# Optimization experiments

Hardware: AMD Instinct MI355X
Metric: run time of the kernel (lower is better)

## Reference

```python
import jax, jax.numpy as jnp
import numpy as np

N = 10000       # nodes
E = 160000      # edges (avg degree 16)
IN_C = 16       # node in_channels
IN_E = 8        # edge in_edge_channels
DIMS = [32, 16, 16, 16]   # hidden_dims
ENN_H = 128     # edge_nn_hidden
EMLP_H = 16     # edge_mlp_hidden


def setup_inputs() -> dict:
    key = jax.random.key(0)
    ks = iter(jax.random.split(key, 80))
    def rn(shape, s=0.1):
        return jax.random.normal(next(ks), shape, dtype=jnp.float32) * s
    inp = {}
    inp['x'] = jax.random.normal(next(ks), (N, IN_C), dtype=jnp.float32)
    inp['edge_attr'] = jax.random.normal(next(ks), (E, IN_E), dtype=jnp.float32)
    inp['edge_index'] = jax.random.randint(next(ks), (2, E), 0, N, dtype=jnp.int32)
    in_dims = [IN_C] + DIMS[:-1]
    for i, (di, do) in enumerate(zip(in_dims, DIMS)):
        inp[f'p_w{i}'] = rn((do, di));            inp[f'p_b{i}'] = rn((do,))
        inp[f'e1_w{i}'] = rn((ENN_H, IN_E));      inp[f'e1_b{i}'] = rn((ENN_H,))
        inp[f'e2_w{i}'] = rn((do * do, ENN_H), 0.02); inp[f'e2_b{i}'] = rn((do * do,), 0.02)
        inp[f'r_w{i}'] = rn((do, do));            inp[f'c_b{i}'] = rn((do,))
    inp['m_w0'] = rn((EMLP_H, DIMS[-1])); inp['m_b0'] = rn((EMLP_H,))
    inp['m_w1'] = rn((1, EMLP_H));        inp['m_b1'] = rn((1,))
    return inp


def _forward(x, edge_attr, edge_index, params, m_w0, m_b0, m_w1, m_b1):
    row, col = edge_index[0], edge_index[1]
    n = x.shape[0]
    # in-degree for scatter-mean (clamped to 1, as PyG scatter mean)
    deg = jnp.clip(jax.ops.segment_sum(jnp.ones(row.shape[0], jnp.float32), col, num_segments=n), 1.0)
    for (pw, pb, ew1, eb1, ew2, eb2, rw, cb) in params:
        d = pw.shape[0]
        x_proj = x @ pw.T + pb                                    # [N, d]
        # edge-conditioned weight matrices: [E, d, d]
        W = (jax.nn.relu(edge_attr @ ew1.T + eb1) @ ew2.T + eb2).reshape(-1, d, d)
        msg = jnp.einsum('ei,eio->eo', x_proj[row], W)            # [E, d]
        agg = jax.ops.segment_sum(msg, col, num_segments=n) / deg[:, None]
        conv = agg + x_proj @ rw.T + cb                           # NNConv: aggr + root + bias
        x = jax.nn.relu(conv) + x_proj                            # relu + skip
    edge_repr = x[row] + x[col]                                   # [E, d_last]
    out = jax.nn.relu(edge_repr @ m_w0.T + m_b0) @ m_w1.T + m_b1  # [E, 1]
    return out[:, 0]


def reference(x, edge_attr, edge_index,
              p_w0, p_b0, e1_w0, e1_b0, e2_w0, e2_b0, r_w0, c_b0,
              p_w1, p_b1, e1_w1, e1_b1, e2_w1, e2_b1, r_w1, c_b1,
              p_w2, p_b2, e1_w2, e1_b2, e2_w2, e2_b2, r_w2, c_b2,
              p_w3, p_b3, e1_w3, e1_b3, e2_w3, e2_b3, r_w3, c_b3,
              m_w0, m_b0, m_w1, m_b1):
    params = [
        (p_w0, p_b0, e1_w0, e1_b0, e2_w0, e2_b0, r_w0, c_b0),
        (p_w1, p_b1, e1_w1, e1_b1, e2_w1, e2_b1, r_w1, c_b1),
        (p_w2, p_b2, e1_w2, e1_b2, e2_w2, e2_b2, r_w2, c_b2),
        (p_w3, p_b3, e1_w3, e1_b3, e2_w3, e2_b3, r_w3, c_b3),
    ]
    return _forward(x, edge_attr, edge_index, params, m_w0, m_b0, m_w1, m_b1)
```

## Files before the change

kernel.cpp:

```cpp
#include <hip/hip_runtime.h>

#define NN 10000
#define NE 160000
static constexpr int TPB = 256;
static constexpr int SCAN_T = 1024;

typedef unsigned int uint32;

static __device__ __forceinline__ ushort f2bf(float f) {
  uint32 u = __float_as_uint(f);
  u += 0x7fff + ((u >> 16) & 1);
  return (ushort)(u >> 16);
}
static __device__ __forceinline__ uint32 pk2bf(float a, float b) {
  return (uint32)f2bf(a) | ((uint32)f2bf(b) << 16);
}
static __device__ __forceinline__ float bflo(uint32 u) {
  return __uint_as_float(u << 16);
}
static __device__ __forceinline__ float bfhi(uint32 u) {
  return __uint_as_float(u & 0xffff0000u);
}
static __device__ __forceinline__ void dot2bf(float& acc, uint32 a, uint32 b) {
  asm("v_dot2_f32_bf16 %0, %1, %2, %0" : "+v"(acc) : "v"(a), "v"(b));
}


__global__ void k_count(const int* __restrict__ ei, int* __restrict__ cnt) {
  int e = blockIdx.x * TPB + threadIdx.x;
  if (e >= NE) return;
  atomicAdd(&cnt[ei[e]], 1);
  atomicAdd(&cnt[NN + ei[NE + e]], 1);
}

__global__ void __launch_bounds__(SCAN_T)
k_scan2(const int* __restrict__ cnt_all, int* __restrict__ off_r, int* __restrict__ cur_r,
        int* __restrict__ off_c, int* __restrict__ cur_c) {
  const int* cnt = (blockIdx.x == 0) ? cnt_all : cnt_all + NN;
  int* off = (blockIdx.x == 0) ? off_r : off_c;
  int* cur = (blockIdx.x == 0) ? cur_r : cur_c;
  __shared__ int s_wave[16];
  __shared__ int s_carry;
  int tid = threadIdx.x;
  int lane = tid & 63, wid = tid >> 6;
  if (tid == 0) s_carry = 0;
  __syncthreads();
  for (int base = 0; base < NN; base += SCAN_T) {
    int i = base + tid;
    int v = (i < NN) ? cnt[i] : 0;
    int s = v;
    #pragma unroll
    for (int d = 1; d < 64; d <<= 1) {
      int t = __shfl_up(s, d, 64);
      if (lane >= d) s += t;
    }
    if (lane == 63) s_wave[wid] = s;
    __syncthreads();
    if (wid == 0 && lane < 16) {
      int ws = s_wave[lane];
      #pragma unroll
      for (int d = 1; d < 16; d <<= 1) {
        int t = __shfl_up(ws, d, 64);
        if (lane >= d) ws += t;
      }
      s_wave[lane] = ws;
    }
    __syncthreads();
    int waveoff = (wid > 0) ? s_wave[wid - 1] : 0;
    int excl = s_carry + waveoff + s - v;
    if (i < NN) { off[i] = excl; cur[i] = excl; }
    __syncthreads();
    if (tid == 0) s_carry += s_wave[15];
    __syncthreads();
  }
  if (tid == 0) off[NN] = s_carry;
}

__global__ void k_fill_row(const int* __restrict__ ei, int* __restrict__ cur_row,
                           int* __restrict__ eid_row) {
  int e = blockIdx.x * TPB + threadIdx.x;
  if (e >= NE) return;
  int r = ei[e];
  int p = atomicAdd(&cur_row[r], 1);
  eid_row[p] = e;
}

__global__ void k_fill_colpos(const int* __restrict__ ei, const int* __restrict__ eid_row,
                              int* __restrict__ cur_col, int* __restrict__ colpos) {
  int s = blockIdx.x * TPB + threadIdx.x;
  if (s >= NE) return;
  int e = eid_row[s];
  int c = ei[NE + e];
  int p = atomicAdd(&cur_col[c], 1);
  colpos[s] = p;
}


template<int DIN, int D>
__global__ void __launch_bounds__(TPB)
k_nodeprep(const float* __restrict__ x, const float* __restrict__ pw, const float* __restrict__ pb,
           const float* __restrict__ rw, const float* __restrict__ cb, const float* __restrict__ eb2,
           float* __restrict__ xp, float* __restrict__ root, float* __restrict__ Bb) {
  __shared__ float s_pw[D * DIN], s_rw[D * D], s_eb2[D * D], s_pb[D], s_cb[D];
  for (int t = threadIdx.x; t < D * DIN; t += TPB) s_pw[t] = pw[t];
  for (int t = threadIdx.x; t < D * D; t += TPB) { s_rw[t] = rw[t]; s_eb2[t] = eb2[t]; }
  for (int t = threadIdx.x; t < D; t += TPB) { s_pb[t] = pb[t]; s_cb[t] = cb[t]; }
  __syncthreads();
  int n = blockIdx.x * TPB + threadIdx.x;
  if (n >= NN) return;
  float xv[DIN];
  const float4* x4 = (const float4*)(x + (size_t)n * DIN);
  #pragma unroll
  for (int i = 0; i < DIN / 4; i++) {
    float4 v = x4[i];
    xv[4*i+0] = v.x; xv[4*i+1] = v.y; xv[4*i+2] = v.z; xv[4*i+3] = v.w;
  }
  float xpv[D];
  #pragma unroll
  for (int o = 0; o < D; o++) {
    float a = s_pb[o];
    #pragma unroll
    for (int i = 0; i < DIN; i++) a = fmaf(s_pw[o*DIN + i], xv[i], a);
    xpv[o] = a;
    xp[(size_t)n*D + o] = a;
  }
  #pragma unroll
  for (int o = 0; o < D; o++) {
    float a = s_cb[o];
    #pragma unroll
    for (int i = 0; i < D; i++) a = fmaf(s_rw[o*D + i], xpv[i], a);
    root[(size_t)n*D + o] = a;
  }
  #pragma unroll
  for (int o = 0; o < D; o++) {
    float a = 0.f;
    #pragma unroll
    for (int i = 0; i < D; i++) a = fmaf(xpv[i], s_eb2[i*D + o], a);
    Bb[(size_t)n*D + o] = a;
  }
}

template<int DP, int D, int NS>
__global__ void __launch_bounds__(TPB)
k_aggprep(const int* __restrict__ col_off,
          const uint32* __restrict__ m0, const uint32* __restrict__ m1,
          const uint32* __restrict__ m2, const uint32* __restrict__ m3,
          const float* __restrict__ root_prev, const float* __restrict__ xp_prev,
          const float* __restrict__ pw, const float* __restrict__ pb,
          const float* __restrict__ rw, const float* __restrict__ cb,
          const float* __restrict__ eb2,
          float* __restrict__ xp, float* __restrict__ root, float* __restrict__ Bb) {
  constexpr int W = DP / 2;
  constexpr int NB = TPB / W;
  __shared__ float s_x[NB][DP];
  __shared__ float s_xpv[NB][D];
  __shared__ float s_pw[D * DP], s_rw[D * D], s_eb2[D * D], s_pb[D], s_cb[D];
  int tid = threadIdx.x;
  for (int t = tid; t < D * DP; t += TPB) s_pw[t] = pw[t];
  for (int t = tid; t < D * D; t += TPB) { s_rw[t] = rw[t]; s_eb2[t] = eb2[t]; }
  for (int t = tid; t < D; t += TPB) { s_pb[t] = pb[t]; s_cb[t] = cb[t]; }
  int g = tid / W, o2 = tid % W;
  int n = blockIdx.x * NB + g;
  if (n < NN) {
    int p0 = col_off[n], p1 = col_off[n + 1];
    float ax = 0.f, ay = 0.f;
    for (int p = p0; p < p1; p++) {
      uint32 w0 = m0[(size_t)p * W + o2];
      uint32 w1 = m1[(size_t)p * W + o2];
      ax += bflo(w0) + bflo(w1);
      ay += bfhi(w0) + bfhi(w1);
      if (NS > 2) {
        uint32 w2 = m2[(size_t)p * W + o2];
        uint32 w3 = m3[(size_t)p * W + o2];
        ax += bflo(w2) + bflo(w3);
        ay += bfhi(w2) + bfhi(w3);
      }
    }
    float deg = (p1 > p0) ? (float)(p1 - p0) : 1.f;
    float2 rp = *(const float2*)(root_prev + (size_t)n * DP + 2 * o2);
    float2 xq = *(const float2*)(xp_prev + (size_t)n * DP + 2 * o2);
    float c0 = ax / deg + rp.x, c1 = ay / deg + rp.y;
    s_x[g][2 * o2]     = (c0 > 0.f ? c0 : 0.f) + xq.x;
    s_x[g][2 * o2 + 1] = (c1 > 0.f ? c1 : 0.f) + xq.y;
  }
  __syncthreads();
  for (int t = tid; t < NB * D; t += TPB) {
    int g2 = t / D, o = t % D;
    int n2 = blockIdx.x * NB + g2;
    if (n2 < NN) {
      float a = s_pb[o];
      #pragma unroll
      for (int i = 0; i < DP; i++) a = fmaf(s_pw[o * DP + i], s_x[g2][i], a);
      s_xpv[g2][o] = a;
      xp[(size_t)n2 * D + o] = a;
    }
  }
  __syncthreads();
  for (int t = tid; t < NB * D; t += TPB) {
    int g2 = t / D, o = t % D;
    int n2 = blockIdx.x * NB + g2;
    if (n2 < NN) {
      float r2 = s_cb[o], b2 = 0.f;
      #pragma unroll
      for (int i = 0; i < D; i++) {
        r2 = fmaf(s_rw[o * D + i], s_xpv[g2][i], r2);
        b2 = fmaf(s_xpv[g2][i], s_eb2[i * D + o], b2);
      }
      root[(size_t)n2 * D + o] = r2;
      Bb[(size_t)n2 * D + o] = b2;
    }
  }
}

__global__ void k_trans_all(const float* __restrict__ e0, const float* __restrict__ e1,
                            const float* __restrict__ e2, const float* __restrict__ e3,
                            uint32* __restrict__ Vp) {
  int t = blockIdx.x * TPB + threadIdx.x;
  const float* ew2; uint32* dst; int D, loc;
  if (t < 65536)       { ew2 = e0; dst = Vp;         D = 32; loc = t; }
  else if (t < 81920)  { ew2 = e1; dst = Vp + 65536; D = 16; loc = t - 65536; }
  else if (t < 98304)  { ew2 = e2; dst = Vp + 81920; D = 16; loc = t - 81920; }
  else if (t < 114688) { ew2 = e3; dst = Vp + 98304; D = 16; loc = t - 98304; }
  else return;
  int COLS = D * 128;
  int i2 = loc / COLS;
  int r = loc - i2 * COLS;
  int w = r >> 1, p = r & 1;
  int k2 = w / D, o = w - k2 * D;
  int k = 2 * k2 + p;
  float lo = ew2[((size_t)((2 * i2) * D + o)) * 128 + k];
  float hi = ew2[((size_t)((2 * i2 + 1) * D + o)) * 128 + k];
  dst[loc] = pk2bf(lo, hi);
}

template<int D, int G, int KS>
__global__ void __launch_bounds__(TPB)
k_fused(const int* __restrict__ eid_row, const int* __restrict__ row_off,
        const int* __restrict__ colpos,
        const float* __restrict__ ea, const float* __restrict__ ew1,
        const float* __restrict__ eb1, const uint32* __restrict__ Vp,
        const float* __restrict__ xp, const float* __restrict__ Bb,
        uint32* __restrict__ m0, uint32* __restrict__ m1,
        uint32* __restrict__ m2, uint32* __restrict__ m3) {
  constexpr int OQ = D / 4;
  constexpr int EB = TPB / OQ;
  constexpr int COLS = D * 128;
  constexpr int UW = COLS / 2;
  constexpr int UH = UW / KS;
  constexpr int UP = UH + 4;
  constexpr int CT = UH / TPB;
  constexpr int KLOC = 128 / KS;
  constexpr int KL2 = KLOC / 2;
  constexpr int HSTR = KL2 + 4;

  __shared__ __align__(16) uint32 s_w1tp[4 * KLOC];
  __shared__ float  s_b1[KLOC];
  __shared__ __align__(16) uint32 s_U[G * UP];
  __shared__ __align__(16) uint32 s_hp[EB * HSTR];
  __shared__ __align__(16) uint32 s_eap[EB * 4];
  __shared__ int    s_cp[EB];
  __shared__ uint32 s_xp2[G][D / 2];
  __shared__ float  s_B[G * D];
  __shared__ int    s_off[G + 1];

  int tid = threadIdx.x;
  int kq = blockIdx.y;
  int n0 = blockIdx.x * G;
  int GA = NN - n0; if (GA > G) GA = G;
  uint32* ms[4] = {m0, m1, m2, m3};
  uint32* msgHp = ms[kq];

  for (int t = tid; t < 4 * KLOC; t += TPB) {
    int i2 = t / KLOC, kloc = t % KLOC;
    int k = kq * KLOC + kloc;
    s_w1tp[t] = pk2bf(ew1[k * 8 + 2 * i2], ew1[k * 8 + 2 * i2 + 1]);
  }
  for (int t = tid; t < KLOC; t += TPB) s_b1[t] = eb1[kq * KLOC + t];
  for (int t = tid; t < G * (D / 2); t += TPB) {
    int g = t / (D / 2), i2 = t % (D / 2);
    if (g < GA) {
      float2 v = *(const float2*)(xp + (size_t)(n0 + g) * D + 2 * i2);
      s_xp2[g][i2] = pk2bf(v.x, v.y);
    } else {
      s_xp2[g][i2] = 0;
    }
  }
  for (int t = tid; t < G * D; t += TPB) {
    int g = t / D, i = t % D;
    s_B[t] = (g < GA && kq == 0) ? Bb[(size_t)(n0 + g) * D + i] : 0.f;
  }
  if (tid <= GA) s_off[tid] = row_off[n0 + tid];
  __syncthreads();

  {
    const uint2* Vp2 = (const uint2*)Vp;
    float accLo[G][CT], accHi[G][CT];
    #pragma unroll
    for (int g = 0; g < G; g++)
      #pragma unroll
      for (int j = 0; j < CT; j++) { accLo[g][j] = 0.f; accHi[g][j] = 0.f; }
    #pragma unroll 2
    for (int i2 = 0; i2 < D / 2; i2++) {
      uint2 vv[CT];
      #pragma unroll
      for (int j = 0; j < CT; j++)
        vv[j] = Vp2[(size_t)i2 * UW + kq * UH + j * TPB + tid];
      #pragma unroll
      for (int g = 0; g < G; g++) {
        uint32 xg = s_xp2[g][i2];
        #pragma unroll
        for (int j = 0; j < CT; j++) {
          dot2bf(accLo[g][j], xg, vv[j].x);
          dot2bf(accHi[g][j], xg, vv[j].y);
        }
      }
    }
    #pragma unroll
    for (int g = 0; g < G; g++)
      #pragma unroll
      for (int j = 0; j < CT; j++)
        s_U[g * UP + j * TPB + tid] = pk2bf(accLo[g][j], accHi[g][j]);
  }

  int p0 = row_off[n0], p1 = row_off[n0 + GA];
  int el = tid / OQ, oq = tid % OQ;
  for (int pc = p0; pc < p1; pc += EB) {
    int cnt = p1 - pc; if (cnt > EB) cnt = EB;
    __syncthreads();
    for (int t = tid; t < cnt * 4; t += TPB) {
      int e2 = t >> 2, i2 = t & 3;
      float2 v = *(const float2*)(ea + (size_t)eid_row[pc + e2] * 8 + 2 * i2);
      s_eap[t] = pk2bf(v.x, v.y);
    }
    for (int t = tid; t < cnt; t += TPB) s_cp[t] = colpos[pc + t];
    __syncthreads();
    for (int t = tid; t < cnt * KL2; t += TPB) {
      int e2 = t / KL2, k2 = t % KL2;
      float a0 = s_b1[2 * k2], a1 = s_b1[2 * k2 + 1];
      #pragma unroll
      for (int i2 = 0; i2 < 4; i2++) {
        uint32 ep = s_eap[e2 * 4 + i2];
        uint2 ww = *(const uint2*)(s_w1tp + i2 * KLOC + 2 * k2);
        dot2bf(a0, ep, ww.x);
        dot2bf(a1, ep, ww.y);
      }
      s_hp[e2 * HSTR + k2] = pk2bf(fmaxf(a0, 0.f), fmaxf(a1, 0.f));
    }
    __syncthreads();
    if (el < cnt) {
      int s = pc + el;
      int g = 0;
      #pragma unroll
      for (int q = 1; q < G; q++) g += (q < GA && s >= s_off[q]) ? 1 : 0;
      const uint32* up = s_U + g * UP + oq * 4;
      const uint32* hp = s_hp + el * HSTR;
      float a0 = 0.f, a1 = 0.f, a2 = 0.f, a3 = 0.f;
      #pragma unroll
      for (int k8 = 0; k8 < KL2 / 4; k8++) {
        uint4 hw = *(const uint4*)(hp + 4 * k8);
        uint4 u0 = *(const uint4*)(up + (4 * k8 + 0) * D);
        uint4 u1 = *(const uint4*)(up + (4 * k8 + 1) * D);
        uint4 u2 = *(const uint4*)(up + (4 * k8 + 2) * D);
        uint4 u3 = *(const uint4*)(up + (4 * k8 + 3) * D);
        dot2bf(a0, hw.x, u0.x); dot2bf(a1, hw.x, u0.y); dot2bf(a2, hw.x, u0.z); dot2bf(a3, hw.x, u0.w);
        dot2bf(a0, hw.y, u1.x); dot2bf(a1, hw.y, u1.y); dot2bf(a2, hw.y, u1.z); dot2bf(a3, hw.y, u1.w);
        dot2bf(a0, hw.z, u2.x); dot2bf(a1, hw.z, u2.y); dot2bf(a2, hw.z, u2.z); dot2bf(a3, hw.z, u2.w);
        dot2bf(a0, hw.w, u3.x); dot2bf(a1, hw.w, u3.y); dot2bf(a2, hw.w, u3.z); dot2bf(a3, hw.w, u3.w);
      }
      float4 b = ((const float4*)(s_B + g * D))[oq];
      uint2 om;
      om.x = pk2bf(a0 + b.x, a1 + b.y);
      om.y = pk2bf(a2 + b.z, a3 + b.w);
      ((uint2*)(msgHp + (size_t)s_cp[el] * (D / 2)))[oq] = om;
    }
  }
}

template<int D, int NS>
__global__ void __launch_bounds__(TPB)
k_agg(const int* __restrict__ col_off,
      const uint32* __restrict__ m0, const uint32* __restrict__ m1,
      const float* __restrict__ root, const float* __restrict__ xp,
      float* __restrict__ xout) {
  constexpr int W = D / 2;
  constexpr int GP = TPB / W;
  int g = threadIdx.x / W, o2 = threadIdx.x % W;
  int n = blockIdx.x * GP + g;
  if (n >= NN) return;
  int p0 = col_off[n], p1 = col_off[n + 1];
  float ax = 0.f, ay = 0.f;
  for (int p = p0; p < p1; p++) {
    uint32 w0 = m0[(size_t)p * W + o2];
    uint32 w1 = m1[(size_t)p * W + o2];
    ax += bflo(w0) + bflo(w1);
    ay += bfhi(w0) + bfhi(w1);
  }
  float deg = (p1 > p0) ? (float)(p1 - p0) : 1.f;
  float2 rp = *(const float2*)(root + (size_t)n * D + 2 * o2);
  float2 xq = *(const float2*)(xp + (size_t)n * D + 2 * o2);
  float c0 = ax / deg + rp.x, c1 = ay / deg + rp.y;
  xout[(size_t)n * D + 2 * o2]     = (c0 > 0.f ? c0 : 0.f) + xq.x;
  xout[(size_t)n * D + 2 * o2 + 1] = (c1 > 0.f ? c1 : 0.f) + xq.y;
}

__global__ void __launch_bounds__(TPB)
k_final(const int* __restrict__ ei, const float* __restrict__ x,
        const float* __restrict__ mw0, const float* __restrict__ mb0,
        const float* __restrict__ mw1, const float* __restrict__ mb1,
        float* __restrict__ out) {
  __shared__ float s_w0[256], s_b0[16], s_w1[16], s_b1;
  for (int t = threadIdx.x; t < 256; t += TPB) s_w0[t] = mw0[t];
  if (threadIdx.x < 16) { s_b0[threadIdx.x] = mb0[threadIdx.x]; s_w1[threadIdx.x] = mw1[threadIdx.x]; }
  if (threadIdx.x == 0) s_b1 = mb1[0];
  __syncthreads();
  int e = blockIdx.x * TPB + threadIdx.x;
  if (e >= NE) return;
  int r = ei[e], c = ei[NE + e];
  const float4* xr4 = (const float4*)(x + (size_t)r * 16);
  const float4* xc4 = (const float4*)(x + (size_t)c * 16);
  float er[16];
  #pragma unroll
  for (int q = 0; q < 4; q++) {
    float4 vr = xr4[q], vc = xc4[q];
    er[4*q+0] = vr.x + vc.x; er[4*q+1] = vr.y + vc.y;
    er[4*q+2] = vr.z + vc.z; er[4*q+3] = vr.w + vc.w;
  }
  float o = s_b1;
  #pragma unroll
  for (int j = 0; j < 16; j++) {
    float t = s_b0[j];
    #pragma unroll
    for (int k = 0; k < 16; k++) t = fmaf(er[k], s_w0[j * 16 + k], t);
    t = fmaxf(t, 0.f);
    o = fmaf(t, s_w1[j], o);
  }
  out[e] = o;
}


struct LayerPtrs {
  const float *pw, *pb, *ew1, *eb1, *ew2, *eb2, *rw, *cb;
};

extern "C" void kernel_launch(void* const* d_in, const int* in_sizes, int n_in,
                              void* d_out, int out_size, void* d_ws, size_t ws_size,
                              hipStream_t stream) {
  (void)in_sizes; (void)n_in; (void)out_size; (void)ws_size;
  const float* x0 = (const float*)d_in[0];
  const float* ea = (const float*)d_in[1];
  const int* ei = (const int*)d_in[2];
  LayerPtrs L[4];
  for (int l = 0; l < 4; l++) {
    L[l].pw  = (const float*)d_in[3 + 8 * l];
    L[l].pb  = (const float*)d_in[4 + 8 * l];
    L[l].ew1 = (const float*)d_in[5 + 8 * l];
    L[l].eb1 = (const float*)d_in[6 + 8 * l];
    L[l].ew2 = (const float*)d_in[7 + 8 * l];
    L[l].eb2 = (const float*)d_in[8 + 8 * l];
    L[l].rw  = (const float*)d_in[9 + 8 * l];
    L[l].cb  = (const float*)d_in[10 + 8 * l];
  }
  const float* mw0 = (const float*)d_in[35];
  const float* mb0 = (const float*)d_in[36];
  const float* mw1 = (const float*)d_in[37];
  const float* mb1 = (const float*)d_in[38];
  float* out = (float*)d_out;

  char* w = (char*)d_ws;
  size_t off = 0;
  auto alloc = [&](size_t b) -> void* {
    void* p = w + off;
    off = (off + b + 255) & ~(size_t)255;
    return p;
  };
  int* cnt      = (int*)alloc(sizeof(int) * 2 * NN);
  int* row_off  = (int*)alloc(sizeof(int) * (NN + 1));
  int* col_off  = (int*)alloc(sizeof(int) * (NN + 1));
  int* cur_row  = (int*)alloc(sizeof(int) * NN);
  int* cur_col  = (int*)alloc(sizeof(int) * NN);
  int* eid_row  = (int*)alloc(sizeof(int) * NE);
  int* colpos   = (int*)alloc(sizeof(int) * NE);
  float* xpA   = (float*)alloc(sizeof(float) * NN * 32);
  float* xpB   = (float*)alloc(sizeof(float) * NN * 32);
  float* rootA = (float*)alloc(sizeof(float) * NN * 32);
  float* rootB = (float*)alloc(sizeof(float) * NN * 32);
  float* Bb    = (float*)alloc(sizeof(float) * NN * 32);
  uint32* msg0 = (uint32*)alloc(sizeof(uint32) * NE * 16);
  uint32* msg1 = (uint32*)alloc(sizeof(uint32) * NE * 16);
  uint32* msg2 = (uint32*)alloc(sizeof(uint32) * NE * 16);
  uint32* msg3 = (uint32*)alloc(sizeof(uint32) * NE * 16);
  float* xfin  = (float*)alloc(sizeof(float) * NN * 16);
  uint32* Vp   = (uint32*)alloc(sizeof(uint32) * 114688);

  hipMemsetAsync(cnt, 0, sizeof(int) * 2 * NN, stream);
  k_count<<<(NE + TPB - 1) / TPB, TPB, 0, stream>>>(ei, cnt);
  k_scan2<<<2, SCAN_T, 0, stream>>>(cnt, row_off, cur_row, col_off, cur_col);
  k_fill_row<<<(NE + TPB - 1) / TPB, TPB, 0, stream>>>(ei, cur_row, eid_row);
  k_fill_colpos<<<(NE + TPB - 1) / TPB, TPB, 0, stream>>>(ei, eid_row, cur_col, colpos);
  k_trans_all<<<(114688 + TPB - 1) / TPB, TPB, 0, stream>>>(
      L[0].ew2, L[1].ew2, L[2].ew2, L[3].ew2, Vp);

  k_nodeprep<16, 32><<<(NN + TPB - 1) / TPB, TPB, 0, stream>>>(
      x0, L[0].pw, L[0].pb, L[0].rw, L[0].cb, L[0].eb2, xpA, rootA, Bb);
  {
    dim3 gf((NN + 5) / 6, 4);
    k_fused<32, 6, 4><<<gf, TPB, 0, stream>>>(
        eid_row, row_off, colpos, ea, L[0].ew1, L[0].eb1, Vp, xpA, Bb,
        msg0, msg1, msg2, msg3);
  }
  k_aggprep<32, 16, 4><<<(NN + 15) / 16, TPB, 0, stream>>>(
      col_off, msg0, msg1, msg2, msg3, rootA, xpA,
      L[1].pw, L[1].pb, L[1].rw, L[1].cb, L[1].eb2, xpB, rootB, Bb);
  {
    dim3 gf((NN + 5) / 6, 2);
    k_fused<16, 6, 2><<<gf, TPB, 0, stream>>>(
        eid_row, row_off, colpos, ea, L[1].ew1, L[1].eb1, Vp + 65536, xpB, Bb,
        msg0, msg1, msg2, msg3);
  }
  k_aggprep<16, 16, 2><<<(NN + 31) / 32, TPB, 0, stream>>>(
      col_off, msg0, msg1, msg2, msg3, rootB, xpB,
      L[2].pw, L[2].pb, L[2].rw, L[2].cb, L[2].eb2, xpA, rootA, Bb);
  {
    dim3 gf((NN + 5) / 6, 2);
    k_fused<16, 6, 2><<<gf, TPB, 0, stream>>>(
        eid_row, row_off, colpos, ea, L[2].ew1, L[2].eb1, Vp + 81920, xpA, Bb,
        msg0, msg1, msg2, msg3);
  }
  k_aggprep<16, 16, 2><<<(NN + 31) / 32, TPB, 0, stream>>>(
      col_off, msg0, msg1, msg2, msg3, rootA, xpA,
      L[3].pw, L[3].pb, L[3].rw, L[3].cb, L[3].eb2, xpB, rootB, Bb);
  {
    dim3 gf((NN + 5) / 6, 2);
    k_fused<16, 6, 2><<<gf, TPB, 0, stream>>>(
        eid_row, row_off, colpos, ea, L[3].ew1, L[3].eb1, Vp + 98304, xpB, Bb,
        msg0, msg1, msg2, msg3);
  }
  k_agg<16, 2><<<(NN + 31) / 32, TPB, 0, stream>>>(
      col_off, msg0, msg1, rootB, xpB, xfin);
  k_final<<<(NE + TPB - 1) / TPB, TPB, 0, stream>>>(ei, xfin, mw0, mb0, mw1, mb1, out);
}
```

Measured before the change: 300.5 us.

## Split edge-MLP hidden computation into a separate kernel writing bf16 hidden to global

```diff
diff --git a/kernel.cpp b/kernel.cpp
--- a/kernel.cpp
+++ b/kernel.cpp
@@ -138,6 +138,54 @@
     for (int i = 0; i < D; i++) a = fmaf(xpv[i], s_eb2[i*D + o], a);
     Bb[(size_t)n*D + o] = a;
   }
+}
+
+__global__ void __launch_bounds__(TPB)
+k_h(const int* __restrict__ eid_row, const float* __restrict__ ea,
+    const float* __restrict__ ew1, const float* __restrict__ eb1,
+    uint32* __restrict__ hg) {
+  __shared__ __align__(16) uint32 s_w[4 * 128];
+  __shared__ float s_b[128];
+  __shared__ uint32 s_ea[32 * 4];
+  int tid = threadIdx.x;
+  for (int t = tid; t < 512; t += TPB) {
+    int i2 = t >> 7, k = t & 127;
+    s_w[t] = pk2bf(ew1[k * 8 + 2 * i2], ew1[k * 8 + 2 * i2 + 1]);
+  }
+  for (int t = tid; t < 128; t += TPB) s_b[t] = eb1[t];
+  int s0 = blockIdx.x * 32;
+  for (int t = tid; t < 32 * 4; t += TPB) {
+    int e2 = t >> 2, i2 = t & 3;
+    int s = s0 + e2;
+    if (s < NE) {
+      float2 v = *(const float2*)(ea + (size_t)eid_row[s] * 8 + 2 * i2);
+      s_ea[t] = pk2bf(v.x, v.y);
+    }
+  }
+  __syncthreads();
+  int e2 = tid >> 3, k8 = tid & 7;
+  int s = s0 + e2;
+  if (s >= NE) return;
+  uint32 ep0 = s_ea[e2 * 4 + 0], ep1 = s_ea[e2 * 4 + 1];
+  uint32 ep2 = s_ea[e2 * 4 + 2], ep3 = s_ea[e2 * 4 + 3];
+  __align__(16) uint32 outw[8];
+  #pragma unroll
+  for (int j = 0; j < 8; j++) {
+    int k2 = k8 * 8 + j;
+    float a0 = s_b[2 * k2], a1 = s_b[2 * k2 + 1];
+    uint2 w0 = *(const uint2*)(s_w + 0 * 128 + 2 * k2);
+    dot2bf(a0, ep0, w0.x); dot2bf(a1, ep0, w0.y);
+    uint2 w1 = *(const uint2*)(s_w + 1 * 128 + 2 * k2);
+    dot2bf(a0, ep1, w1.x); dot2bf(a1, ep1, w1.y);
+    uint2 w2 = *(const uint2*)(s_w + 2 * 128 + 2 * k2);
+    dot2bf(a0, ep2, w2.x); dot2bf(a1, ep2, w2.y);
+    uint2 w3 = *(const uint2*)(s_w + 3 * 128 + 2 * k2);
+    dot2bf(a0, ep3, w3.x); dot2bf(a1, ep3, w3.y);
+    outw[j] = pk2bf(fmaxf(a0, 0.f), fmaxf(a1, 0.f));
+  }
+  uint4* dst = (uint4*)(hg + (size_t)s * 64 + k8 * 8);
+  dst[0] = *(uint4*)&outw[0];
+  dst[1] = *(uint4*)&outw[4];
 }
 
 template<int DP, int D, int NS>
@@ -235,10 +283,8 @@
 
 template<int D, int G, int KS>
 __global__ void __launch_bounds__(TPB)
-k_fused(const int* __restrict__ eid_row, const int* __restrict__ row_off,
-        const int* __restrict__ colpos,
-        const float* __restrict__ ea, const float* __restrict__ ew1,
-        const float* __restrict__ eb1, const uint32* __restrict__ Vp,
+k_fused(const int* __restrict__ row_off, const int* __restrict__ colpos,
+        const uint32* __restrict__ hg, const uint32* __restrict__ Vp,
         const float* __restrict__ xp, const float* __restrict__ Bb,
         uint32* __restrict__ m0, uint32* __restrict__ m1,
         uint32* __restrict__ m2, uint32* __restrict__ m3) {
@@ -249,16 +295,9 @@
   constexpr int UH = UW / KS;
   constexpr int UP = UH + 4;
   constexpr int CT = UH / TPB;
-  constexpr int KLOC = 128 / KS;
-  constexpr int KL2 = KLOC / 2;
-  constexpr int HSTR = KL2 + 4;
-
-  __shared__ __align__(16) uint32 s_w1tp[4 * KLOC];
-  __shared__ float  s_b1[KLOC];
+  constexpr int KL2 = 64 / KS;
+
   __shared__ __align__(16) uint32 s_U[G * UP];
-  __shared__ __align__(16) uint32 s_hp[EB * HSTR];
-  __shared__ __align__(16) uint32 s_eap[EB * 4];
-  __shared__ int    s_cp[EB];
   __shared__ uint32 s_xp2[G][D / 2];
   __shared__ float  s_B[G * D];
   __shared__ int    s_off[G + 1];
@@ -270,12 +309,6 @@
   uint32* ms[4] = {m0, m1, m2, m3};
   uint32* msgHp = ms[kq];
 
-  for (int t = tid; t < 4 * KLOC; t += TPB) {
-    int i2 = t / KLOC, kloc = t % KLOC;
-    int k = kq * KLOC + kloc;
-    s_w1tp[t] = pk2bf(ew1[k * 8 + 2 * i2], ew1[k * 8 + 2 * i2 + 1]);
-  }
-  for (int t = tid; t < KLOC; t += TPB) s_b1[t] = eb1[kq * KLOC + t];
   for (int t = tid; t < G * (D / 2); t += TPB) {
     int g = t / (D / 2), i2 = t % (D / 2);
     if (g < GA) {
@@ -321,58 +354,34 @@
       for (int j = 0; j < CT; j++)
         s_U[g * UP + j * TPB + tid] = pk2bf(accLo[g][j], accHi[g][j]);
   }
-
-  int p0 = row_off[n0], p1 = row_off[n0 + GA];
+  __syncthreads();
+
+  int p0 = s_off[0], p1 = s_off[GA];
   int el = tid / OQ, oq = tid % OQ;
-  for (int pc = p0; pc < p1; pc += EB) {
-    int cnt = p1 - pc; if (cnt > EB) cnt = EB;
-    __syncthreads();
-    for (int t = tid; t < cnt * 4; t += TPB) {
-      int e2 = t >> 2, i2 = t & 3;
-      float2 v = *(const float2*)(ea + (size_t)eid_row[pc + e2] * 8 + 2 * i2);
-      s_eap[t] = pk2bf(v.x, v.y);
-    }
-    for (int t = tid; t < cnt; t += TPB) s_cp[t] = colpos[pc + t];
-    __syncthreads();
-    for (int t = tid; t < cnt * KL2; t += TPB) {
-      int e2 = t / KL2, k2 = t % KL2;
-      float a0 = s_b1[2 * k2], a1 = s_b1[2 * k2 + 1];
-      #pragma unroll
-      for (int i2 = 0; i2 < 4; i2++) {
-        uint32 ep = s_eap[e2 * 4 + i2];
-        uint2 ww = *(const uint2*)(s_w1tp + i2 * KLOC + 2 * k2);
-        dot2bf(a0, ep, ww.x);
-        dot2bf(a1, ep, ww.y);
-      }
-      s_hp[e2 * HSTR + k2] = pk2bf(fmaxf(a0, 0.f), fmaxf(a1, 0.f));
-    }
-    __syncthreads();
-    if (el < cnt) {
-      int s = pc + el;
-      int g = 0;
-      #pragma unroll
-      for (int q = 1; q < G; q++) g += (q < GA && s >= s_off[q]) ? 1 : 0;
-      const uint32* up = s_U + g * UP + oq * 4;
-      const uint32* hp = s_hp + el * HSTR;
-      float a0 = 0.f, a1 = 0.f, a2 = 0.f, a3 = 0.f;
-      #pragma unroll
-      for (int k8 = 0; k8 < KL2 / 4; k8++) {
-        uint4 hw = *(const uint4*)(hp + 4 * k8);
-        uint4 u0 = *(const uint4*)(up + (4 * k8 + 0) * D);
-        uint4 u1 = *(const uint4*)(up + (4 * k8 + 1) * D);
-        uint4 u2 = *(const uint4*)(up + (4 * k8 + 2) * D);
-        uint4 u3 = *(const uint4*)(up + (4 * k8 + 3) * D);
-        dot2bf(a0, hw.x, u0.x); dot2bf(a1, hw.x, u0.y); dot2bf(a2, hw.x, u0.z); dot2bf(a3, hw.x, u0.w);
-        dot2bf(a0, hw.y, u1.x); dot2bf(a1, hw.y, u1.y); dot2bf(a2, hw.y, u1.z); dot2bf(a3, hw.y, u1.w);
-        dot2bf(a0, hw.z, u2.x); dot2bf(a1, hw.z, u2.y); dot2bf(a2, hw.z, u2.z); dot2bf(a3, hw.z, u2.w);
-        dot2bf(a0, hw.w, u3.x); dot2bf(a1, hw.w, u3.y); dot2bf(a2, hw.w, u3.z); dot2bf(a3, hw.w, u3.w);
-      }
-      float4 b = ((const float4*)(s_B + g * D))[oq];
-      uint2 om;
-      om.x = pk2bf(a0 + b.x, a1 + b.y);
-      om.y = pk2bf(a2 + b.z, a3 + b.w);
-      ((uint2*)(msgHp + (size_t)s_cp[el] * (D / 2)))[oq] = om;
-    }
+  for (int s = p0 + el; s < p1; s += EB) {
+    int g = 0;
+    #pragma unroll
+    for (int q = 1; q < G; q++) g += (q < GA && s >= s_off[q]) ? 1 : 0;
+    const uint32* hp = hg + (size_t)s * 64 + kq * KL2;
+    const uint32* up = s_U + g * UP + oq * 4;
+    float a0 = 0.f, a1 = 0.f, a2 = 0.f, a3 = 0.f;
+    #pragma unroll
+    for (int k8 = 0; k8 < KL2 / 4; k8++) {
+      uint4 hw = *(const uint4*)(hp + 4 * k8);
+      uint4 u0 = *(const uint4*)(up + (4 * k8 + 0) * D);
+      uint4 u1 = *(const uint4*)(up + (4 * k8 + 1) * D);
+      uint4 u2 = *(const uint4*)(up + (4 * k8 + 2) * D);
+      uint4 u3 = *(const uint4*)(up + (4 * k8 + 3) * D);
+      dot2bf(a0, hw.x, u0.x); dot2bf(a1, hw.x, u0.y); dot2bf(a2, hw.x, u0.z); dot2bf(a3, hw.x, u0.w);
+      dot2bf(a0, hw.y, u1.x); dot2bf(a1, hw.y, u1.y); dot2bf(a2, hw.y, u1.z); dot2bf(a3, hw.y, u1.w);
+      dot2bf(a0, hw.z, u2.x); dot2bf(a1, hw.z, u2.y); dot2bf(a2, hw.z, u2.z); dot2bf(a3, hw.z, u2.w);
+      dot2bf(a0, hw.w, u3.x); dot2bf(a1, hw.w, u3.y); dot2bf(a2, hw.w, u3.z); dot2bf(a3, hw.w, u3.w);
+    }
+    float4 b = ((const float4*)(s_B + g * D))[oq];
+    uint2 om;
+    om.x = pk2bf(a0 + b.x, a1 + b.y);
+    om.y = pk2bf(a2 + b.z, a3 + b.w);
+    ((uint2*)(msgHp + (size_t)colpos[s] * (D / 2)))[oq] = om;
   }
 }
 
@@ -489,6 +498,7 @@
   uint32* msg1 = (uint32*)alloc(sizeof(uint32) * NE * 16);
   uint32* msg2 = (uint32*)alloc(sizeof(uint32) * NE * 16);
   uint32* msg3 = (uint32*)alloc(sizeof(uint32) * NE * 16);
+  uint32* hg   = (uint32*)alloc(sizeof(uint32) * (size_t)NE * 64);
   float* xfin  = (float*)alloc(sizeof(float) * NN * 16);
   uint32* Vp   = (uint32*)alloc(sizeof(uint32) * 114688);
 
@@ -500,40 +510,41 @@
   k_trans_all<<<(114688 + TPB - 1) / TPB, TPB, 0, stream>>>(
       L[0].ew2, L[1].ew2, L[2].ew2, L[3].ew2, Vp);
 
+  const int HB = (NE + 31) / 32;
   k_nodeprep<16, 32><<<(NN + TPB - 1) / TPB, TPB, 0, stream>>>(
       x0, L[0].pw, L[0].pb, L[0].rw, L[0].cb, L[0].eb2, xpA, rootA, Bb);
+  k_h<<<HB, TPB, 0, stream>>>(eid_row, ea, L[0].ew1, L[0].eb1, hg);
   {
     dim3 gf((NN + 5) / 6, 4);
     k_fused<32, 6, 4><<<gf, TPB, 0, stream>>>(
-        eid_row, row_off, colpos, ea, L[0].ew1, L[0].eb1, Vp, xpA, Bb,
-        msg0, msg1, msg2, msg3);
+        row_off, colpos, hg, Vp, xpA, Bb, msg0, msg1, msg2, msg3);
   }
   k_aggprep<32, 16, 4><<<(NN + 15) / 16, TPB, 0, stream>>>(
       col_off, msg0, msg1, msg2, msg3, rootA, xpA,
       L[1].pw, L[1].pb, L[1].rw, L[1].cb, L[1].eb2, xpB, rootB, Bb);
+  k_h<<<HB, TPB, 0, stream>>>(eid_row, ea, L[1].ew1, L[1].eb1, hg);
   {
     dim3 gf((NN + 5) / 6, 2);
     k_fused<16, 6, 2><<<gf, TPB, 0, stream>>>(
-        eid_row, row_off, colpos, ea, L[1].ew1, L[1].eb1, Vp + 65536, xpB, Bb,
-        msg0, msg1, msg2, msg3);
+        row_off, colpos, hg, Vp + 65536, xpB, Bb, msg0, msg1, msg2, msg3);
   }
   k_aggprep<16, 16, 2><<<(NN + 31) / 32, TPB, 0, stream>>>(
       col_off, msg0, msg1, msg2, msg3, rootB, xpB,
       L[2].pw, L[2].pb, L[2].rw, L[2].cb, L[2].eb2, xpA, rootA, Bb);
+  k_h<<<HB, TPB, 0, stream>>>(eid_row, ea, L[2].ew1, L[2].eb1, hg);
   {
     dim3 gf((NN + 5) / 6, 2);
     k_fused<16, 6, 2><<<gf, TPB, 0, stream>>>(
-        eid_row, row_off, colpos, ea, L[2].ew1, L[2].eb1, Vp + 81920, xpA, Bb,
-        msg0, msg1, msg2, msg3);
+        row_off, colpos, hg, Vp + 81920, xpA, Bb, msg0, msg1, msg2, msg3);
   }
   k_aggprep<16, 16, 2><<<(NN + 31) / 32, TPB, 0, stream>>>(
       col_off, msg0, msg1, msg2, msg3, rootA, xpA,
       L[3].pw, L[3].pb, L[3].rw, L[3].cb, L[3].eb2, xpB, rootB, Bb);
+  k_h<<<HB, TPB, 0, stream>>>(eid_row, ea, L[3].ew1, L[3].eb1, hg);
   {
     dim3 gf((NN + 5) / 6, 2);
     k_fused<16, 6, 2><<<gf, TPB, 0, stream>>>(
-        eid_row, row_off, colpos, ea, L[3].ew1, L[3].eb1, Vp + 98304, xpB, Bb,
-        msg0, msg1, msg2, msg3);
+        row_off, colpos, hg, Vp + 98304, xpB, Bb, msg0, msg1, msg2, msg3);
   }
   k_agg<16, 2><<<(NN + 31) / 32, TPB, 0, stream>>>(
       col_off, msg0, msg1, rootB, xpB, xfin);
```

Measured after the change: 363.7 us. 21.0% more time.
